# Optimization experiments

Hardware: AMD Instinct MI355X
Metric: run time of the kernel (lower is better)

The kernel has to match this reference:

```python
import jax, jax.numpy as jnp
import numpy as np

N_NODES = 10000
N_EDGES = 320000
N_GRAPHS = 16


def _sage_layer(h, src, dst, W_self, W_neigh, b):
    # DGL SAGEConv('mean'): out_i = h_i @ W_self + mean_{j in N_in(i)} h_j @ W_neigh + b
    msg_sum = jax.ops.segment_sum(h[src], dst, num_segments=N_NODES)
    deg = jax.ops.segment_sum(jnp.ones(src.shape[0], h.dtype), dst, num_segments=N_NODES)
    h_neigh = msg_sum / jnp.maximum(deg, 1.0)[:, None]
    return h @ W_self + h_neigh @ W_neigh + b


def _segment_mean(x, seg, num_segments):
    s = jax.ops.segment_sum(x, seg, num_segments=num_segments)
    c = jax.ops.segment_sum(jnp.ones(x.shape[0], x.dtype), seg, num_segments=num_segments)
    return s / jnp.maximum(c, 1.0)[:, None]


def setup_inputs() -> dict:
    key = jax.random.key(0)
    ks = jax.random.split(key, 16)
    d_in, d_h, n_cls = 256, 64, 2

    def glorot(k, shape):
        fan_in = shape[0]
        return jax.random.normal(k, shape, dtype=jnp.float32) / np.sqrt(fan_in)

    return {
        "feat": jax.random.normal(ks[0], (N_NODES, d_in), dtype=jnp.float32),
        "src": jax.random.randint(ks[1], (N_EDGES,), 0, N_NODES),
        "dst": jax.random.randint(ks[2], (N_EDGES,), 0, N_NODES),
        "graph_id": jnp.sort(jax.random.randint(ks[3], (N_NODES,), 0, N_GRAPHS)),
        "W_self1": glorot(ks[4], (d_in, d_h)),
        "W_neigh1": glorot(ks[5], (d_in, d_h)),
        "b1": jnp.zeros((d_h,), jnp.float32),
        "W_self2": glorot(ks[6], (d_h, d_h)),
        "W_neigh2": glorot(ks[7], (d_h, d_h)),
        "b2": jnp.zeros((d_h,), jnp.float32),
        "W_self3": glorot(ks[8], (d_h, d_h)),
        "W_neigh3": glorot(ks[9], (d_h, d_h)),
        "b3": jnp.zeros((d_h,), jnp.float32),
        "W_cls": glorot(ks[10], (d_h, n_cls)),
        "b_cls": jnp.zeros((n_cls,), jnp.float32),
    }


def reference(feat, src, dst, graph_id, W_self1, W_neigh1, b1, W_self2, W_neigh2, b2,
              W_self3, W_neigh3, b3, W_cls, b_cls):
    # layer 1 + relu (dropout is identity in eval mode)
    h = jax.nn.relu(_sage_layer(feat, src, dst, W_self1, W_neigh1, b1))
    # layer 2 + relu
    h = jax.nn.relu(_sage_layer(h, src, dst, W_self2, W_neigh2, b2))
    # layer 3 (no activation)
    h = _sage_layer(h, src, dst, W_self3, W_neigh3, b3)
    # dgl.mean_nodes readout per graph
    out_feat = _segment_mean(h, graph_id, N_GRAPHS)
    out = out_feat @ W_cls + b_cls
    return (out, out_feat, h)
```

## Files before the change

kernel.cpp:

```cpp
#include <hip/hip_runtime.h>


#define DH 64
#define NG 16
#define NSB 8
#define DTILES 32
#define MAXNPB 1250
#define CAP 32
#define TILE_F 4352

__device__ __forceinline__ unsigned short f2bf(float f) {
    unsigned int u = __float_as_uint(f);
    unsigned int r = (u + 0x7FFFu + ((u >> 16) & 1u)) >> 16;
    return (unsigned short)r;
}
__device__ __forceinline__ float bfu(unsigned short v) {
    return __uint_as_float(((unsigned int)v) << 16);
}

__global__ __launch_bounds__(512) void gemm1_build_kernel(
    const float* __restrict__ X, const float* __restrict__ Ws_g,
    const float* __restrict__ Wn_g, const float* __restrict__ bias,
    float* __restrict__ S, unsigned short* __restrict__ P,
    const int* __restrict__ src, const int* __restrict__ dst,
    int* __restrict__ cnt8, unsigned short* __restrict__ es16,
    int M, int E, int npb8, int gb) {
    constexpr int K = 256;
    int tid = threadIdx.x;

    if ((int)blockIdx.x >= gb) {
        int i = ((int)blockIdx.x - gb) * 512 + tid;
        if (i < E) {
            int s = src[i];
            int b = s / npb8;
            int k = dst[i] * NSB + b;
            int p = atomicAdd(&cnt8[k], 1);
            if (p < CAP)
                es16[(size_t)k * CAP + p] = (unsigned short)(s - b * npb8);
        }
        return;
    }

    __shared__ float smem[6 * TILE_F];
    const int grp = tid >> 8;
    const int t   = tid & 255;
    const int cx = t & 15;
    const int ry = t >> 4;
    float* Xs  = smem + grp * 3 * TILE_F;
    float* Wsm = Xs + TILE_F;
    float* Wnm = Wsm + TILE_F;
    const int row0 = blockIdx.x * 64;
    float4 acc_s[4] = {{0.f,0.f,0.f,0.f},{0.f,0.f,0.f,0.f},
                       {0.f,0.f,0.f,0.f},{0.f,0.f,0.f,0.f}};
    float4 acc_n[4] = {{0.f,0.f,0.f,0.f},{0.f,0.f,0.f,0.f},
                       {0.f,0.f,0.f,0.f},{0.f,0.f,0.f,0.f}};

    for (int st = 0; st < 2; ++st) {
        const int kc = grp * 128 + st * 64;
#pragma unroll
        for (int it = 0; it < 4; ++it) {
            int q = t + 256 * it;
            int row = q >> 4;
            int k4 = (q & 15) * 4;
            float4 xv = make_float4(0.f, 0.f, 0.f, 0.f);
            int gr = row0 + row;
            if (gr < M)
                xv = *reinterpret_cast<const float4*>(&X[(size_t)gr * K + kc + k4]);
            *reinterpret_cast<float4*>(&Xs[row * 68 + k4]) = xv;
            *reinterpret_cast<float4*>(&Wsm[row * 68 + k4]) =
                *reinterpret_cast<const float4*>(&Ws_g[(size_t)(kc + row) * 64 + k4]);
            *reinterpret_cast<float4*>(&Wnm[row * 68 + k4]) =
                *reinterpret_cast<const float4*>(&Wn_g[(size_t)(kc + row) * 64 + k4]);
        }
        __syncthreads();
#pragma unroll 4
        for (int kk = 0; kk < 64; ++kk) {
            float av[4];
#pragma unroll
            for (int j = 0; j < 4; ++j) av[j] = Xs[(ry * 4 + j) * 68 + kk];
            float4 bs4 = *reinterpret_cast<const float4*>(&Wsm[kk * 68 + cx * 4]);
            float4 bn4 = *reinterpret_cast<const float4*>(&Wnm[kk * 68 + cx * 4]);
#pragma unroll
            for (int j = 0; j < 4; ++j) {
                acc_s[j].x += av[j] * bs4.x; acc_s[j].y += av[j] * bs4.y;
                acc_s[j].z += av[j] * bs4.z; acc_s[j].w += av[j] * bs4.w;
                acc_n[j].x += av[j] * bn4.x; acc_n[j].y += av[j] * bn4.y;
                acc_n[j].z += av[j] * bn4.z; acc_n[j].w += av[j] * bn4.w;
            }
        }
        __syncthreads();
    }

    float* flat = smem + 3 * TILE_F;
    if (grp == 1) {
        int o = t * 33;
#pragma unroll
        for (int j = 0; j < 4; ++j) {
            flat[o + j * 4 + 0] = acc_s[j].x; flat[o + j * 4 + 1] = acc_s[j].y;
            flat[o + j * 4 + 2] = acc_s[j].z; flat[o + j * 4 + 3] = acc_s[j].w;
            flat[o + 16 + j * 4 + 0] = acc_n[j].x; flat[o + 16 + j * 4 + 1] = acc_n[j].y;
            flat[o + 16 + j * 4 + 2] = acc_n[j].z; flat[o + 16 + j * 4 + 3] = acc_n[j].w;
        }
    }
    __syncthreads();
    if (grp == 0) {
        int o = t * 33;
        int col = cx * 4;
        float4 b4 = *reinterpret_cast<const float4*>(&bias[col]);
#pragma unroll
        for (int j = 0; j < 4; ++j) {
            acc_s[j].x += flat[o + j * 4 + 0]; acc_s[j].y += flat[o + j * 4 + 1];
            acc_s[j].z += flat[o + j * 4 + 2]; acc_s[j].w += flat[o + j * 4 + 3];
            acc_n[j].x += flat[o + 16 + j * 4 + 0]; acc_n[j].y += flat[o + 16 + j * 4 + 1];
            acc_n[j].z += flat[o + 16 + j * 4 + 2]; acc_n[j].w += flat[o + 16 + j * 4 + 3];
            int r = row0 + ry * 4 + j;
            if (r < M) {
                float4 sv;
                sv.x = acc_s[j].x + b4.x; sv.y = acc_s[j].y + b4.y;
                sv.z = acc_s[j].z + b4.z; sv.w = acc_s[j].w + b4.w;
                *reinterpret_cast<float4*>(&S[(size_t)r * DH + col]) = sv;
                ushort4 pk;
                pk.x = f2bf(acc_n[j].x); pk.y = f2bf(acc_n[j].y);
                pk.z = f2bf(acc_n[j].z); pk.w = f2bf(acc_n[j].w);
                *reinterpret_cast<ushort4*>(&P[(size_t)r * DH + col]) = pk;
            }
        }
    }
}

__global__ __launch_bounds__(512) void gemm_dual_kernel(
    const float* __restrict__ X, const float* __restrict__ Ws_g,
    const float* __restrict__ Wn_g, const float* __restrict__ bias,
    const float* __restrict__ Hn_part, const int* __restrict__ cnt8,
    float* __restrict__ S, unsigned short* __restrict__ P, int M) {
    constexpr int K = 64;
    __shared__ float smem[3 * TILE_F];
    int tid = threadIdx.x;
    const int grp = tid >> 8;
    const int t   = tid & 255;
    const int cx = t & 15;
    const int ry = t >> 4;
    float* Xs  = smem;
    float* Wsm = smem + TILE_F;
    float* Wnm = smem + 2 * TILE_F;
    const int row0 = blockIdx.x * 64;
    float4 acc_s[4] = {{0.f,0.f,0.f,0.f},{0.f,0.f,0.f,0.f},
                       {0.f,0.f,0.f,0.f},{0.f,0.f,0.f,0.f}};
    float4 acc_n[4] = {{0.f,0.f,0.f,0.f},{0.f,0.f,0.f,0.f},
                       {0.f,0.f,0.f,0.f},{0.f,0.f,0.f,0.f}};

    {
#pragma unroll
        for (int it = 0; it < 2; ++it) {
            int q = tid + 512 * it;
            int row = q >> 4;
            int k4 = (q & 15) * 4;
            float4 xv = make_float4(0.f, 0.f, 0.f, 0.f);
            int gr = row0 + row;
            if (gr < M) {
                xv = *reinterpret_cast<const float4*>(&X[(size_t)gr * K + k4]);
                const int4* cp = reinterpret_cast<const int4*>(&cnt8[gr * NSB]);
                int4 c0 = cp[0], c1 = cp[1];
                int ca[8] = {c0.x, c0.y, c0.z, c0.w, c1.x, c1.y, c1.z, c1.w};
                int deg = ca[0] + ca[1] + ca[2] + ca[3] +
                          ca[4] + ca[5] + ca[6] + ca[7];
                float4 pv[8];
                size_t pb = (size_t)gr * NSB * DH + k4;
#pragma unroll
                for (int b = 0; b < NSB; ++b)
                    pv[b] = *reinterpret_cast<const float4*>(&Hn_part[pb + b * DH]);
                float4 hv = make_float4(0.f, 0.f, 0.f, 0.f);
#pragma unroll
                for (int b = 0; b < NSB; ++b) {
                    bool use = ca[b] > 0;
                    hv.x += use ? pv[b].x : 0.f;
                    hv.y += use ? pv[b].y : 0.f;
                    hv.z += use ? pv[b].z : 0.f;
                    hv.w += use ? pv[b].w : 0.f;
                }
                float inv = 1.f / fmaxf((float)deg, 1.f);
                xv.x = fmaxf(fmaf(hv.x, inv, xv.x), 0.f);
                xv.y = fmaxf(fmaf(hv.y, inv, xv.y), 0.f);
                xv.z = fmaxf(fmaf(hv.z, inv, xv.z), 0.f);
                xv.w = fmaxf(fmaf(hv.w, inv, xv.w), 0.f);
            }
            *reinterpret_cast<float4*>(&Xs[row * 68 + k4]) = xv;
            *reinterpret_cast<float4*>(&Wsm[row * 68 + k4]) =
                *reinterpret_cast<const float4*>(&Ws_g[(size_t)row * 64 + k4]);
            *reinterpret_cast<float4*>(&Wnm[row * 68 + k4]) =
                *reinterpret_cast<const float4*>(&Wn_g[(size_t)row * 64 + k4]);
        }
        __syncthreads();
        const int kk0 = grp * 32;
#pragma unroll 4
        for (int kk = kk0; kk < kk0 + 32; ++kk) {
            float av[4];
#pragma unroll
            for (int j = 0; j < 4; ++j) av[j] = Xs[(ry * 4 + j) * 68 + kk];
            float4 bs4 = *reinterpret_cast<const float4*>(&Wsm[kk * 68 + cx * 4]);
            float4 bn4 = *reinterpret_cast<const float4*>(&Wnm[kk * 68 + cx * 4]);
#pragma unroll
            for (int j = 0; j < 4; ++j) {
                acc_s[j].x += av[j] * bs4.x; acc_s[j].y += av[j] * bs4.y;
                acc_s[j].z += av[j] * bs4.z; acc_s[j].w += av[j] * bs4.w;
                acc_n[j].x += av[j] * bn4.x; acc_n[j].y += av[j] * bn4.y;
                acc_n[j].z += av[j] * bn4.z; acc_n[j].w += av[j] * bn4.w;
            }
        }
        __syncthreads();
    }

    if (grp == 1) {
        int o = t * 33;
#pragma unroll
        for (int j = 0; j < 4; ++j) {
            smem[o + j * 4 + 0] = acc_s[j].x; smem[o + j * 4 + 1] = acc_s[j].y;
            smem[o + j * 4 + 2] = acc_s[j].z; smem[o + j * 4 + 3] = acc_s[j].w;
            smem[o + 16 + j * 4 + 0] = acc_n[j].x; smem[o + 16 + j * 4 + 1] = acc_n[j].y;
            smem[o + 16 + j * 4 + 2] = acc_n[j].z; smem[o + 16 + j * 4 + 3] = acc_n[j].w;
        }
    }
    __syncthreads();
    if (grp == 0) {
        int o = t * 33;
        int col = cx * 4;
        float4 b4 = *reinterpret_cast<const float4*>(&bias[col]);
#pragma unroll
        for (int j = 0; j < 4; ++j) {
            acc_s[j].x += smem[o + j * 4 + 0]; acc_s[j].y += smem[o + j * 4 + 1];
            acc_s[j].z += smem[o + j * 4 + 2]; acc_s[j].w += smem[o + j * 4 + 3];
            acc_n[j].x += smem[o + 16 + j * 4 + 0]; acc_n[j].y += smem[o + 16 + j * 4 + 1];
            acc_n[j].z += smem[o + 16 + j * 4 + 2]; acc_n[j].w += smem[o + 16 + j * 4 + 3];
            int r = row0 + ry * 4 + j;
            if (r < M) {
                float4 sv;
                sv.x = acc_s[j].x + b4.x; sv.y = acc_s[j].y + b4.y;
                sv.z = acc_s[j].z + b4.z; sv.w = acc_s[j].w + b4.w;
                *reinterpret_cast<float4*>(&S[(size_t)r * DH + col]) = sv;
                ushort4 pk;
                pk.x = f2bf(acc_n[j].x); pk.y = f2bf(acc_n[j].y);
                pk.z = f2bf(acc_n[j].z); pk.w = f2bf(acc_n[j].w);
                *reinterpret_cast<ushort4*>(&P[(size_t)r * DH + col]) = pk;
            }
        }
    }
}

__global__ __launch_bounds__(1024) void agg_kernel(
    const unsigned short* __restrict__ P, const int* __restrict__ cnt8,
    const unsigned short* __restrict__ es16, float* __restrict__ Hn_part,
    int M, int npb8) {
    __shared__ __align__(16) unsigned short sP[MAXNPB * DH];
    int tid = threadIdx.x;
    int sb    = blockIdx.x & (NSB - 1);
    int dtile = blockIdx.x >> 3;
    int s0 = sb * npb8;
    int snodes = min(npb8, M - s0);

    {
        const uint4* gp = reinterpret_cast<const uint4*>(P + (size_t)s0 * DH);
        int cnt = snodes * 8;
        for (int j = tid; j < cnt; j += 1024)
            *reinterpret_cast<uint4*>(&sP[j * 8]) = gp[j];
    }
    __syncthreads();

    int lane = tid & 63, wid = tid >> 6;
    int dpb  = (M + DTILES - 1) / DTILES;
    int d0t  = dtile * dpb;
    int dend = min(d0t + dpb, M);

    for (int dstn = d0t + wid; dstn < dend; dstn += 16) {
        int key = dstn * NSB + sb;
        int cnt = min(cnt8[key], CAP);
        if (cnt == 0) continue;
        size_t base = (size_t)key * CAP;
        float acc = 0.f;
        int cmax = cnt - 1;
        for (int e = 0; e < cnt; e += 4) {
            int i0 = es16[base + min(e + 0, cmax)];
            int i1 = es16[base + min(e + 1, cmax)];
            int i2 = es16[base + min(e + 2, cmax)];
            int i3 = es16[base + min(e + 3, cmax)];
            float m1 = (e + 1 < cnt) ? 1.f : 0.f;
            float m2 = (e + 2 < cnt) ? 1.f : 0.f;
            float m3 = (e + 3 < cnt) ? 1.f : 0.f;
            float f0 = bfu(sP[(size_t)i0 * DH + lane]);
            float f1 = bfu(sP[(size_t)i1 * DH + lane]);
            float f2 = bfu(sP[(size_t)i2 * DH + lane]);
            float f3 = bfu(sP[(size_t)i3 * DH + lane]);
            acc += f0;
            acc = fmaf(m1, f1, acc);
            acc = fmaf(m2, f2, acc);
            acc = fmaf(m3, f3, acc);
        }
        Hn_part[(size_t)key * DH + lane] = acc;
    }
}

__global__ __launch_bounds__(256) void finish_readout_kernel(
    const float* __restrict__ S, const float* __restrict__ Hn_part,
    const int* __restrict__ cnt8, const int* __restrict__ graph_id,
    float* __restrict__ H, float* __restrict__ gsum, float* __restrict__ gcnt,
    const float* __restrict__ Wc, const float* __restrict__ bc,
    float* __restrict__ out, float* __restrict__ out_feat,
    unsigned int* __restrict__ done, int M, int fb) {
    int tid  = threadIdx.x;
    int lane = tid & 63;
    int wv   = tid >> 6;
    {
        int wid = blockIdx.x * 4 + wv;
        int nw  = fb * 4;
        int cpw = (M + nw - 1) / nw;
        int n0 = wid * cpw, n1 = min(n0 + cpw, M);
        if (n0 < n1) {
            float acc = 0.f;
            int cnt = 0;
            int cur = graph_id[n0];
            for (int n = n0; n < n1; ++n) {
                int gid = graph_id[n];
                if (gid != cur) {
                    atomicAdd(&gsum[cur * DH + lane], acc);
                    if (lane == 0) atomicAdd(&gcnt[cur], (float)cnt);
                    acc = 0.f; cnt = 0; cur = gid;
                }
                const int4* cp = reinterpret_cast<const int4*>(&cnt8[n * NSB]);
                int4 c0 = cp[0], c1 = cp[1];
                int ca[8] = {c0.x, c0.y, c0.z, c0.w, c1.x, c1.y, c1.z, c1.w};
                int deg = ca[0] + ca[1] + ca[2] + ca[3] +
                          ca[4] + ca[5] + ca[6] + ca[7];
                float pv[8];
                size_t pb = (size_t)n * NSB * DH + lane;
#pragma unroll
                for (int b = 0; b < NSB; ++b) pv[b] = Hn_part[pb + b * DH];
                float hn = 0.f;
#pragma unroll
                for (int b = 0; b < NSB; ++b) hn += (ca[b] > 0) ? pv[b] : 0.f;
                float inv = 1.f / fmaxf((float)deg, 1.f);
                size_t o = (size_t)n * DH + lane;
                float val = fmaf(hn, inv, S[o]);
                H[o] = val;
                acc += val;
                ++cnt;
            }
            atomicAdd(&gsum[cur * DH + lane], acc);
            if (lane == 0) atomicAdd(&gcnt[cur], (float)cnt);
        }
    }

    __shared__ unsigned int s_ticket;
    __syncthreads();
    if (tid == 0) {
        __threadfence();
        s_ticket = __hip_atomic_fetch_add(done, 1u, __ATOMIC_ACQ_REL,
                                          __HIP_MEMORY_SCOPE_AGENT);
    }
    __syncthreads();
    if (s_ticket != (unsigned int)(fb - 1)) return;
    if (tid == 0) __threadfence();
    __syncthreads();

    __shared__ float ofs[NG][DH];
#pragma unroll
    for (int q = 0; q < 4; ++q) {
        int idx = tid + 256 * q;
        int g = idx >> 6, d = idx & 63;
        float of = gsum[idx] / fmaxf(gcnt[g], 1.0f);
        out_feat[idx] = of;
        ofs[g][d] = of;
    }
    __syncthreads();
    if (tid < NG * 2) {
        int gg = tid >> 1, cc = tid & 1;
        float accv = bc[cc];
#pragma unroll 8
        for (int dd = 0; dd < DH; ++dd) accv += ofs[gg][dd] * Wc[dd * 2 + cc];
        out[gg * 2 + cc] = accv;
    }
}

extern "C" void kernel_launch(void* const* d_in, const int* in_sizes, int n_in,
                              void* d_out, int out_size, void* d_ws, size_t ws_size,
                              hipStream_t stream) {
    const float* feat     = (const float*)d_in[0];
    const int*   src      = (const int*)d_in[1];
    const int*   dst      = (const int*)d_in[2];
    const int*   graph_id = (const int*)d_in[3];
    const float* Ws1 = (const float*)d_in[4];
    const float* Wn1 = (const float*)d_in[5];
    const float* b1  = (const float*)d_in[6];
    const float* Ws2 = (const float*)d_in[7];
    const float* Wn2 = (const float*)d_in[8];
    const float* b2  = (const float*)d_in[9];
    const float* Ws3 = (const float*)d_in[10];
    const float* Wn3 = (const float*)d_in[11];
    const float* b3  = (const float*)d_in[12];
    const float* Wc  = (const float*)d_in[13];
    const float* bc  = (const float*)d_in[14];

    const int M  = in_sizes[3];
    const int E  = in_sizes[1];
    const int M2 = M * NSB;
    const int npb8 = (M + NSB - 1) / NSB;

    float* out      = (float*)d_out;
    float* out_feat = out + NG * 2;
    float* Hbuf     = out_feat + NG * DH;

    char* w = (char*)d_ws;
    size_t off = 0;
    auto carve = [&](size_t bytes) {
        size_t o = off;
        off = (off + bytes + 255) & ~(size_t)255;
        return o;
    };
    int*   cnt8  = (int*)  (w + carve((size_t)M2 * 4));
    float* gsum  = (float*)(w + carve((size_t)NG * DH * 4));
    float* gcnt  = (float*)(w + carve((size_t)NG * 4));
    unsigned int* done = (unsigned int*)(w + carve(4));
    size_t zero_bytes = off;
    unsigned short* es16 = (unsigned short*)(w + carve((size_t)M2 * CAP * 2));
    float* Sbuf  = (float*)(w + carve((size_t)M * DH * 4));
    unsigned short* Pbuf = (unsigned short*)(w + carve((size_t)M * DH * 2));
    float* Hn_part = (float*)(w + carve((size_t)M2 * DH * 4));
    (void)ws_size; (void)n_in; (void)out_size;

    (void)hipMemsetAsync(d_ws, 0, zero_bytes, stream);

    int gb = (M + 63) / 64;
    int eb = (E + 511) / 512;
    int ab = NSB * DTILES;
    int fb = 320;

    gemm1_build_kernel<<<gb + eb, 512, 0, stream>>>(
        feat, Ws1, Wn1, b1, Sbuf, Pbuf,
        src, dst, cnt8, es16, M, E, npb8, gb);
    agg_kernel<<<ab, 1024, 0, stream>>>(Pbuf, cnt8, es16, Hn_part, M, npb8);

    gemm_dual_kernel<<<gb, 512, 0, stream>>>(
        Sbuf, Ws2, Wn2, b2, Hn_part, cnt8, Sbuf, Pbuf, M);
    agg_kernel<<<ab, 1024, 0, stream>>>(Pbuf, cnt8, es16, Hn_part, M, npb8);

    gemm_dual_kernel<<<gb, 512, 0, stream>>>(
        Sbuf, Ws3, Wn3, b3, Hn_part, cnt8, Sbuf, Pbuf, M);
    agg_kernel<<<ab, 1024, 0, stream>>>(Pbuf, cnt8, es16, Hn_part, M, npb8);

    finish_readout_kernel<<<fb, 256, 0, stream>>>(
        Sbuf, Hn_part, cnt8, graph_id, Hbuf, gsum, gcnt,
        Wc, bc, out, out_feat, done, M, fb);
}
```

Before: 234.9 us.

## Shrink GEMM tiles to 16 rows per 256-thread block and share one templated body

The layer-1 and layer-2/3 GEMM kernels now use one templated helper that processes 16 rows per block, with 256 threads and one row of 4 output columns per thread. The old version used 64-row tiles, 512 threads and a split-K reduction through shared memory. The new layout launches about four times as many blocks, which should fill the GPU's compute units and removes the cross-group reduction pass. In exchange, each block reloads the full weight matrices into shared memory, and each weight value read from shared memory now feeds only one row's FMAs. The edge-bucketing part of the fused layer-1 kernel is resized to 256 threads to match.

```diff
diff --git a/kernel.cpp b/kernel.cpp
--- a/kernel.cpp
+++ b/kernel.cpp
@@ -7,7 +7,9 @@
 #define DTILES 32
 #define MAXNPB 1250
 #define CAP 32
-#define TILE_F 4352
+#define GROWS 16
+#define XS_F  1088
+#define W_F   4352
 
 __device__ __forceinline__ unsigned short f2bf(float f) {
     unsigned int u = __float_as_uint(f);
@@ -18,18 +20,107 @@
     return __uint_as_float(((unsigned int)v) << 16);
 }
 
-__global__ __launch_bounds__(512) void gemm1_build_kernel(
+template <int K, bool FUSE>
+__device__ __forceinline__ void gemm_tile16(
+    const float* __restrict__ X, const float* __restrict__ Ws_g,
+    const float* __restrict__ Wn_g, const float* __restrict__ bias,
+    const float* __restrict__ Hn_part, const int* __restrict__ cnt8,
+    float* __restrict__ S, unsigned short* __restrict__ P,
+    int M, int tile, float* smem) {
+    float* Xs  = smem;
+    float* Wsm = smem + XS_F;
+    float* Wnm = Wsm + W_F;
+    const int t   = threadIdx.x;
+    const int cx  = t & 15;
+    const int row = t >> 4;
+    const int row0 = tile * GROWS;
+    float4 acc_s = make_float4(0.f, 0.f, 0.f, 0.f);
+    float4 acc_n = make_float4(0.f, 0.f, 0.f, 0.f);
+
+    for (int kc = 0; kc < K; kc += 64) {
+        {
+            int k4 = cx * 4;
+            int gr = row0 + row;
+            float4 xv = make_float4(0.f, 0.f, 0.f, 0.f);
+            if (gr < M) {
+                xv = *reinterpret_cast<const float4*>(&X[(size_t)gr * K + kc + k4]);
+                if constexpr (FUSE) {
+                    const int4* cp = reinterpret_cast<const int4*>(&cnt8[gr * NSB]);
+                    int4 c0 = cp[0], c1 = cp[1];
+                    int ca[8] = {c0.x, c0.y, c0.z, c0.w, c1.x, c1.y, c1.z, c1.w};
+                    int deg = ca[0] + ca[1] + ca[2] + ca[3] +
+                              ca[4] + ca[5] + ca[6] + ca[7];
+                    float4 pv[8];
+                    size_t pb = (size_t)gr * NSB * DH + k4;
+#pragma unroll
+                    for (int b = 0; b < NSB; ++b)
+                        pv[b] = *reinterpret_cast<const float4*>(&Hn_part[pb + b * DH]);
+                    float4 hv = make_float4(0.f, 0.f, 0.f, 0.f);
+#pragma unroll
+                    for (int b = 0; b < NSB; ++b) {
+                        bool use = ca[b] > 0;
+                        hv.x += use ? pv[b].x : 0.f;
+                        hv.y += use ? pv[b].y : 0.f;
+                        hv.z += use ? pv[b].z : 0.f;
+                        hv.w += use ? pv[b].w : 0.f;
+                    }
+                    float inv = 1.f / fmaxf((float)deg, 1.f);
+                    xv.x = fmaxf(fmaf(hv.x, inv, xv.x), 0.f);
+                    xv.y = fmaxf(fmaf(hv.y, inv, xv.y), 0.f);
+                    xv.z = fmaxf(fmaf(hv.z, inv, xv.z), 0.f);
+                    xv.w = fmaxf(fmaf(hv.w, inv, xv.w), 0.f);
+                }
+            }
+            *reinterpret_cast<float4*>(&Xs[row * 68 + k4]) = xv;
+        }
+#pragma unroll
+        for (int it = 0; it < 4; ++it) {
+            int q = t + 256 * it;
+            int wr = q >> 4;
+            int k4 = (q & 15) * 4;
+            *reinterpret_cast<float4*>(&Wsm[wr * 68 + k4]) =
+                *reinterpret_cast<const float4*>(&Ws_g[(size_t)(kc + wr) * 64 + k4]);
+            *reinterpret_cast<float4*>(&Wnm[wr * 68 + k4]) =
+                *reinterpret_cast<const float4*>(&Wn_g[(size_t)(kc + wr) * 64 + k4]);
+        }
+        __syncthreads();
+#pragma unroll 8
+        for (int kk = 0; kk < 64; ++kk) {
+            float a = Xs[row * 68 + kk];
+            float4 bs4 = *reinterpret_cast<const float4*>(&Wsm[kk * 68 + cx * 4]);
+            float4 bn4 = *reinterpret_cast<const float4*>(&Wnm[kk * 68 + cx * 4]);
+            acc_s.x += a * bs4.x; acc_s.y += a * bs4.y;
+            acc_s.z += a * bs4.z; acc_s.w += a * bs4.w;
+            acc_n.x += a * bn4.x; acc_n.y += a * bn4.y;
+            acc_n.z += a * bn4.z; acc_n.w += a * bn4.w;
+        }
+        __syncthreads();
+    }
+
+    int r = row0 + row;
+    if (r < M) {
+        int col = cx * 4;
+        float4 b4 = *reinterpret_cast<const float4*>(&bias[col]);
+        float4 sv;
+        sv.x = acc_s.x + b4.x; sv.y = acc_s.y + b4.y;
+        sv.z = acc_s.z + b4.z; sv.w = acc_s.w + b4.w;
+        *reinterpret_cast<float4*>(&S[(size_t)r * DH + col]) = sv;
+        ushort4 pk;
+        pk.x = f2bf(acc_n.x); pk.y = f2bf(acc_n.y);
+        pk.z = f2bf(acc_n.z); pk.w = f2bf(acc_n.w);
+        *reinterpret_cast<ushort4*>(&P[(size_t)r * DH + col]) = pk;
+    }
+}
+
+__global__ __launch_bounds__(256) void gemm1_build_kernel(
     const float* __restrict__ X, const float* __restrict__ Ws_g,
     const float* __restrict__ Wn_g, const float* __restrict__ bias,
     float* __restrict__ S, unsigned short* __restrict__ P,
     const int* __restrict__ src, const int* __restrict__ dst,
     int* __restrict__ cnt8, unsigned short* __restrict__ es16,
     int M, int E, int npb8, int gb) {
-    constexpr int K = 256;
-    int tid = threadIdx.x;
-
     if ((int)blockIdx.x >= gb) {
-        int i = ((int)blockIdx.x - gb) * 512 + tid;
+        int i = ((int)blockIdx.x - gb) * 256 + threadIdx.x;
         if (i < E) {
             int s = src[i];
             int b = s / npb8;
@@ -40,210 +131,19 @@
         }
         return;
     }
-
-    __shared__ float smem[6 * TILE_F];
-    const int grp = tid >> 8;
-    const int t   = tid & 255;
-    const int cx = t & 15;
-    const int ry = t >> 4;
-    float* Xs  = smem + grp * 3 * TILE_F;
-    float* Wsm = Xs + TILE_F;
-    float* Wnm = Wsm + TILE_F;
-    const int row0 = blockIdx.x * 64;
-    float4 acc_s[4] = {{0.f,0.f,0.f,0.f},{0.f,0.f,0.f,0.f},
-                       {0.f,0.f,0.f,0.f},{0.f,0.f,0.f,0.f}};
-    float4 acc_n[4] = {{0.f,0.f,0.f,0.f},{0.f,0.f,0.f,0.f},
-                       {0.f,0.f,0.f,0.f},{0.f,0.f,0.f,0.f}};
-
-    for (int st = 0; st < 2; ++st) {
-        const int kc = grp * 128 + st * 64;
-#pragma unroll
-        for (int it = 0; it < 4; ++it) {
-            int q = t + 256 * it;
-            int row = q >> 4;
-            int k4 = (q & 15) * 4;
-            float4 xv = make_float4(0.f, 0.f, 0.f, 0.f);
-            int gr = row0 + row;
-            if (gr < M)
-                xv = *reinterpret_cast<const float4*>(&X[(size_t)gr * K + kc + k4]);
-            *reinterpret_cast<float4*>(&Xs[row * 68 + k4]) = xv;
-            *reinterpret_cast<float4*>(&Wsm[row * 68 + k4]) =
-                *reinterpret_cast<const float4*>(&Ws_g[(size_t)(kc + row) * 64 + k4]);
-            *reinterpret_cast<float4*>(&Wnm[row * 68 + k4]) =
-                *reinterpret_cast<const float4*>(&Wn_g[(size_t)(kc + row) * 64 + k4]);
-        }
-        __syncthreads();
-#pragma unroll 4
-        for (int kk = 0; kk < 64; ++kk) {
-            float av[4];
-#pragma unroll
-            for (int j = 0; j < 4; ++j) av[j] = Xs[(ry * 4 + j) * 68 + kk];
-            float4 bs4 = *reinterpret_cast<const float4*>(&Wsm[kk * 68 + cx * 4]);
-            float4 bn4 = *reinterpret_cast<const float4*>(&Wnm[kk * 68 + cx * 4]);
-#pragma unroll
-            for (int j = 0; j < 4; ++j) {
-                acc_s[j].x += av[j] * bs4.x; acc_s[j].y += av[j] * bs4.y;
-                acc_s[j].z += av[j] * bs4.z; acc_s[j].w += av[j] * bs4.w;
-                acc_n[j].x += av[j] * bn4.x; acc_n[j].y += av[j] * bn4.y;
-                acc_n[j].z += av[j] * bn4.z; acc_n[j].w += av[j] * bn4.w;
-            }
-        }
-        __syncthreads();
-    }
-
-    float* flat = smem + 3 * TILE_F;
-    if (grp == 1) {
-        int o = t * 33;
-#pragma unroll
-        for (int j = 0; j < 4; ++j) {
-            flat[o + j * 4 + 0] = acc_s[j].x; flat[o + j * 4 + 1] = acc_s[j].y;
-            flat[o + j * 4 + 2] = acc_s[j].z; flat[o + j * 4 + 3] = acc_s[j].w;
-            flat[o + 16 + j * 4 + 0] = acc_n[j].x; flat[o + 16 + j * 4 + 1] = acc_n[j].y;
-            flat[o + 16 + j * 4 + 2] = acc_n[j].z; flat[o + 16 + j * 4 + 3] = acc_n[j].w;
-        }
-    }
-    __syncthreads();
-    if (grp == 0) {
-        int o = t * 33;
-        int col = cx * 4;
-        float4 b4 = *reinterpret_cast<const float4*>(&bias[col]);
-#pragma unroll
-        for (int j = 0; j < 4; ++j) {
-            acc_s[j].x += flat[o + j * 4 + 0]; acc_s[j].y += flat[o + j * 4 + 1];
-            acc_s[j].z += flat[o + j * 4 + 2]; acc_s[j].w += flat[o + j * 4 + 3];
-            acc_n[j].x += flat[o + 16 + j * 4 + 0]; acc_n[j].y += flat[o + 16 + j * 4 + 1];
-            acc_n[j].z += flat[o + 16 + j * 4 + 2]; acc_n[j].w += flat[o + 16 + j * 4 + 3];
-            int r = row0 + ry * 4 + j;
-            if (r < M) {
-                float4 sv;
-                sv.x = acc_s[j].x + b4.x; sv.y = acc_s[j].y + b4.y;
-                sv.z = acc_s[j].z + b4.z; sv.w = acc_s[j].w + b4.w;
-                *reinterpret_cast<float4*>(&S[(size_t)r * DH + col]) = sv;
-                ushort4 pk;
-                pk.x = f2bf(acc_n[j].x); pk.y = f2bf(acc_n[j].y);
-                pk.z = f2bf(acc_n[j].z); pk.w = f2bf(acc_n[j].w);
-                *reinterpret_cast<ushort4*>(&P[(size_t)r * DH + col]) = pk;
-            }
-        }
-    }
-}
-
-__global__ __launch_bounds__(512) void gemm_dual_kernel(
+    __shared__ float smem[XS_F + 2 * W_F];
+    gemm_tile16<256, false>(X, Ws_g, Wn_g, bias, nullptr, nullptr,
+                            S, P, M, blockIdx.x, smem);
+}
+
+__global__ __launch_bounds__(256) void gemm_dual_kernel(
     const float* __restrict__ X, const float* __restrict__ Ws_g,
     const float* __restrict__ Wn_g, const float* __restrict__ bias,
     const float* __restrict__ Hn_part, const int* __restrict__ cnt8,
     float* __restrict__ S, unsigned short* __restrict__ P, int M) {
-    constexpr int K = 64;
-    __shared__ float smem[3 * TILE_F];
-    int tid = threadIdx.x;
-    const int grp = tid >> 8;
-    const int t   = tid & 255;
-    const int cx = t & 15;
-    const int ry = t >> 4;
-    float* Xs  = smem;
-    float* Wsm = smem + TILE_F;
-    float* Wnm = smem + 2 * TILE_F;
-    const int row0 = blockIdx.x * 64;
-    float4 acc_s[4] = {{0.f,0.f,0.f,0.f},{0.f,0.f,0.f,0.f},
-                       {0.f,0.f,0.f,0.f},{0.f,0.f,0.f,0.f}};
-    float4 acc_n[4] = {{0.f,0.f,0.f,0.f},{0.f,0.f,0.f,0.f},
-                       {0.f,0.f,0.f,0.f},{0.f,0.f,0.f,0.f}};
-
-    {
-#pragma unroll
-        for (int it = 0; it < 2; ++it) {
-            int q = tid + 512 * it;
-            int row = q >> 4;
-            int k4 = (q & 15) * 4;
-            float4 xv = make_float4(0.f, 0.f, 0.f, 0.f);
-            int gr = row0 + row;
-            if (gr < M) {
-                xv = *reinterpret_cast<const float4*>(&X[(size_t)gr * K + k4]);
-                const int4* cp = reinterpret_cast<const int4*>(&cnt8[gr * NSB]);
-                int4 c0 = cp[0], c1 = cp[1];
-                int ca[8] = {c0.x, c0.y, c0.z, c0.w, c1.x, c1.y, c1.z, c1.w};
-                int deg = ca[0] + ca[1] + ca[2] + ca[3] +
-                          ca[4] + ca[5] + ca[6] + ca[7];
-                float4 pv[8];
-                size_t pb = (size_t)gr * NSB * DH + k4;
-#pragma unroll
-                for (int b = 0; b < NSB; ++b)
-                    pv[b] = *reinterpret_cast<const float4*>(&Hn_part[pb + b * DH]);
-                float4 hv = make_float4(0.f, 0.f, 0.f, 0.f);
-#pragma unroll
-                for (int b = 0; b < NSB; ++b) {
-                    bool use = ca[b] > 0;
-                    hv.x += use ? pv[b].x : 0.f;
-                    hv.y += use ? pv[b].y : 0.f;
-                    hv.z += use ? pv[b].z : 0.f;
-                    hv.w += use ? pv[b].w : 0.f;
-                }
-                float inv = 1.f / fmaxf((float)deg, 1.f);
-                xv.x = fmaxf(fmaf(hv.x, inv, xv.x), 0.f);
-                xv.y = fmaxf(fmaf(hv.y, inv, xv.y), 0.f);
-                xv.z = fmaxf(fmaf(hv.z, inv, xv.z), 0.f);
-                xv.w = fmaxf(fmaf(hv.w, inv, xv.w), 0.f);
-            }
-            *reinterpret_cast<float4*>(&Xs[row * 68 + k4]) = xv;
-            *reinterpret_cast<float4*>(&Wsm[row * 68 + k4]) =
-                *reinterpret_cast<const float4*>(&Ws_g[(size_t)row * 64 + k4]);
-            *reinterpret_cast<float4*>(&Wnm[row * 68 + k4]) =
-                *reinterpret_cast<const float4*>(&Wn_g[(size_t)row * 64 + k4]);
-        }
-        __syncthreads();
-        const int kk0 = grp * 32;
-#pragma unroll 4
-        for (int kk = kk0; kk < kk0 + 32; ++kk) {
-            float av[4];
-#pragma unroll
-            for (int j = 0; j < 4; ++j) av[j] = Xs[(ry * 4 + j) * 68 + kk];
-            float4 bs4 = *reinterpret_cast<const float4*>(&Wsm[kk * 68 + cx * 4]);
-            float4 bn4 = *reinterpret_cast<const float4*>(&Wnm[kk * 68 + cx * 4]);
-#pragma unroll
-            for (int j = 0; j < 4; ++j) {
-                acc_s[j].x += av[j] * bs4.x; acc_s[j].y += av[j] * bs4.y;
-                acc_s[j].z += av[j] * bs4.z; acc_s[j].w += av[j] * bs4.w;
-                acc_n[j].x += av[j] * bn4.x; acc_n[j].y += av[j] * bn4.y;
-                acc_n[j].z += av[j] * bn4.z; acc_n[j].w += av[j] * bn4.w;
-            }
-        }
-        __syncthreads();
-    }
-
-    if (grp == 1) {
-        int o = t * 33;
-#pragma unroll
-        for (int j = 0; j < 4; ++j) {
-            smem[o + j * 4 + 0] = acc_s[j].x; smem[o + j * 4 + 1] = acc_s[j].y;
-            smem[o + j * 4 + 2] = acc_s[j].z; smem[o + j * 4 + 3] = acc_s[j].w;
-            smem[o + 16 + j * 4 + 0] = acc_n[j].x; smem[o + 16 + j * 4 + 1] = acc_n[j].y;
-            smem[o + 16 + j * 4 + 2] = acc_n[j].z; smem[o + 16 + j * 4 + 3] = acc_n[j].w;
-        }
-    }
-    __syncthreads();
-    if (grp == 0) {
-        int o = t * 33;
-        int col = cx * 4;
-        float4 b4 = *reinterpret_cast<const float4*>(&bias[col]);
-#pragma unroll
-        for (int j = 0; j < 4; ++j) {
-            acc_s[j].x += smem[o + j * 4 + 0]; acc_s[j].y += smem[o + j * 4 + 1];
-            acc_s[j].z += smem[o + j * 4 + 2]; acc_s[j].w += smem[o + j * 4 + 3];
-            acc_n[j].x += smem[o + 16 + j * 4 + 0]; acc_n[j].y += smem[o + 16 + j * 4 + 1];
-            acc_n[j].z += smem[o + 16 + j * 4 + 2]; acc_n[j].w += smem[o + 16 + j * 4 + 3];
-            int r = row0 + ry * 4 + j;
-            if (r < M) {
-                float4 sv;
-                sv.x = acc_s[j].x + b4.x; sv.y = acc_s[j].y + b4.y;
-                sv.z = acc_s[j].z + b4.z; sv.w = acc_s[j].w + b4.w;
-                *reinterpret_cast<float4*>(&S[(size_t)r * DH + col]) = sv;
-                ushort4 pk;
-                pk.x = f2bf(acc_n[j].x); pk.y = f2bf(acc_n[j].y);
-                pk.z = f2bf(acc_n[j].z); pk.w = f2bf(acc_n[j].w);
-                *reinterpret_cast<ushort4*>(&P[(size_t)r * DH + col]) = pk;
-            }
-        }
-    }
+    __shared__ float smem[XS_F + 2 * W_F];
+    gemm_tile16<64, true>(X, Ws_g, Wn_g, bias, Hn_part, cnt8,
+                          S, P, M, blockIdx.x, smem);
 }
 
 __global__ __launch_bounds__(1024) void agg_kernel(
@@ -427,21 +327,21 @@
 
     (void)hipMemsetAsync(d_ws, 0, zero_bytes, stream);
 
-    int gb = (M + 63) / 64;
-    int eb = (E + 511) / 512;
+    int gb = (M + GROWS - 1) / GROWS;
+    int eb = (E + 255) / 256;
     int ab = NSB * DTILES;
     int fb = 320;
 
-    gemm1_build_kernel<<<gb + eb, 512, 0, stream>>>(
+    gemm1_build_kernel<<<gb + eb, 256, 0, stream>>>(
         feat, Ws1, Wn1, b1, Sbuf, Pbuf,
         src, dst, cnt8, es16, M, E, npb8, gb);
     agg_kernel<<<ab, 1024, 0, stream>>>(Pbuf, cnt8, es16, Hn_part, M, npb8);
 
-    gemm_dual_kernel<<<gb, 512, 0, stream>>>(
+    gemm_dual_kernel<<<gb, 256, 0, stream>>>(
         Sbuf, Ws2, Wn2, b2, Hn_part, cnt8, Sbuf, Pbuf, M);
     agg_kernel<<<ab, 1024, 0, stream>>>(Pbuf, cnt8, es16, Hn_part, M, npb8);
 
-    gemm_dual_kernel<<<gb, 512, 0, stream>>>(
+    gemm_dual_kernel<<<gb, 256, 0, stream>>>(
         Sbuf, Ws3, Wn3, b3, Hn_part, cnt8, Sbuf, Pbuf, M);
     agg_kernel<<<ab, 1024, 0, stream>>>(Pbuf, cnt8, es16, Hn_part, M, npb8);
 
```

New measurement: 236.0 us. About the same (+0.5%).
